# Kernel optimization log

Measured on AMD Instinct MI355X. Metric: run time of the kernel, lower is better.

The kernel has to match this reference:

```python
import jax, jax.numpy as jnp
import numpy as np

B, S, D_IN, D_OUT = 4, 2048, 2048, 8192


def setup_inputs() -> dict:
    key = jax.random.key(0)
    k1, k2 = jax.random.split(key)
    x = jax.random.normal(k1, (B, S, D_IN), dtype=jnp.float32)
    weight = jax.random.normal(k2, (D_OUT, D_IN), dtype=jnp.float32) * 0.02
    alpha = jnp.float32(1.0)
    bias = jnp.zeros((D_OUT,), dtype=jnp.float32)
    return {"x": x, "weight": weight, "alpha": alpha, "bias": bias}


def reference(x, weight, alpha, bias):
    # Ternary quantization: delta = 0.7 * mean(|w|); w_q in {-1,0,1} * alpha
    delta = 0.7 * jnp.mean(jnp.abs(weight))
    w_t = jnp.where(weight > delta, jnp.float32(1.0),
                    jnp.where(weight < -delta, jnp.float32(-1.0), jnp.float32(0.0)))
    w_q = w_t * alpha  # [out, in]
    # F.linear: x @ w_q^T + bias
    return jnp.einsum('bsd,od->bso', x, w_q) + bias
```

## Files before the change

### kernel.cpp

```cpp
#include <hip/hip_runtime.h>
#include <hip/hip_bf16.h>
#include <stdint.h>

typedef __attribute__((ext_vector_type(4))) int i32x4;
typedef __attribute__((ext_vector_type(16))) int i32x16;
typedef signed char s8;

#define M_TOT 8192
#define N_TOT 8192
#define K_TOT 2048
#define W_COUNT (N_TOT * K_TOT)
#define X_COUNT (M_TOT * K_TOT)

__global__ void tl_reduce(const float* __restrict__ w, const float* __restrict__ x,
                          double* __restrict__ wsum, float* __restrict__ xmax) {
    const int b = blockIdx.x;
    if (b < 1024) {
        const int tid = b * 256 + threadIdx.x;
        const float4* w4 = (const float4*)w;
        double s = 0.0;
        for (int i = tid; i < W_COUNT / 4; i += 1024 * 256) {
            float4 v = w4[i];
            s += (double)fabsf(v.x) + (double)fabsf(v.y) + (double)fabsf(v.z) + (double)fabsf(v.w);
        }
        #pragma unroll
        for (int off = 32; off > 0; off >>= 1) s += __shfl_down(s, off);
        __shared__ double red[4];
        if ((threadIdx.x & 63) == 0) red[threadIdx.x >> 6] = s;
        __syncthreads();
        if (threadIdx.x == 0) wsum[b] = (red[0] + red[1]) + (red[2] + red[3]);
    } else {
        const int tid = (b - 1024) * 256 + threadIdx.x;
        const float4* x4 = (const float4*)x;
        float m = 0.0f;
        for (int i = tid; i < X_COUNT / 4; i += 1024 * 256) {
            float4 v = x4[i];
            m = fmaxf(m, fmaxf(fmaxf(fabsf(v.x), fabsf(v.y)), fmaxf(fabsf(v.z), fabsf(v.w))));
        }
        #pragma unroll
        for (int off = 32; off > 0; off >>= 1) m = fmaxf(m, __shfl_down(m, off));
        __shared__ float redm[4];
        if ((threadIdx.x & 63) == 0) redm[threadIdx.x >> 6] = m;
        __syncthreads();
        if (threadIdx.x == 0) xmax[b - 1024] = fmaxf(fmaxf(redm[0], redm[1]), fmaxf(redm[2], redm[3]));
    }
}

__global__ void tl_finalize(const double* __restrict__ wsum, const float* __restrict__ xmax,
                            const float* __restrict__ alpha,
                            double* __restrict__ delta, float* __restrict__ qp) {
    const int t = threadIdx.x;
    double s = (wsum[t] + wsum[t + 256]) + (wsum[t + 512] + wsum[t + 768]);
    float m = fmaxf(fmaxf(xmax[t], xmax[t + 256]), fmaxf(xmax[t + 512], xmax[t + 768]));
    #pragma unroll
    for (int off = 32; off > 0; off >>= 1) {
        s += __shfl_down(s, off);
        m = fmaxf(m, __shfl_down(m, off));
    }
    __shared__ double rs[4];
    __shared__ float rm[4];
    if ((t & 63) == 0) { rs[t >> 6] = s; rm[t >> 6] = m; }
    __syncthreads();
    if (t == 0) {
        *delta = 0.7 * (((rs[0] + rs[1]) + (rs[2] + rs[3])) / (double)W_COUNT);
        float mm = fmaxf(fmaxf(rm[0], rm[1]), fmaxf(rm[2], rm[3]));
        qp[0] = 127.0f / mm;
        qp[1] = alpha[0] * (mm / 127.0f);
    }
}

__global__ void tl_tern_w(const float* __restrict__ w, const double* __restrict__ delta_p,
                          s8* __restrict__ wb) {
    const double d = *delta_p;
    const int i = (blockIdx.x * 256 + threadIdx.x) * 16;
    union { s8 c[16]; i32x4 v; } o;
    #pragma unroll
    for (int j = 0; j < 16; j += 4) {
        float4 v = *(const float4*)(w + i + j);
        float f[4] = {v.x, v.y, v.z, v.w};
        #pragma unroll
        for (int r = 0; r < 4; ++r) {
            double wd = (double)f[r];
            o.c[j + r] = wd > d ? 1 : (wd < -d ? -1 : 0);
        }
    }
    *(i32x4*)(wb + i) = o.v;
}

__global__ void tl_quant_x(const float* __restrict__ x, const float* __restrict__ qp,
                           s8* __restrict__ xb) {
    const float inv = qp[0];
    const int i = (blockIdx.x * 256 + threadIdx.x) * 16;
    union { s8 c[16]; i32x4 v; } o;
    #pragma unroll
    for (int j = 0; j < 16; j += 4) {
        float4 v = *(const float4*)(x + i + j);
        float f[4] = {v.x, v.y, v.z, v.w};
        #pragma unroll
        for (int r = 0; r < 4; ++r) {
            int q = (int)__builtin_rintf(f[r] * inv);
            q = q > 127 ? 127 : (q < -127 ? -127 : q);
            o.c[j + r] = (s8)q;
        }
    }
    *(i32x4*)(xb + i) = o.v;
}


#define SB    __builtin_amdgcn_sched_barrier(0)
#define BARR  __builtin_amdgcn_s_barrier()
#define LGKM6 asm volatile("s_waitcnt lgkmcnt(6)" ::: "memory")
#define LGKM0 asm volatile("s_waitcnt lgkmcnt(0)" ::: "memory")
#define VMW(N) asm volatile("s_waitcnt vmcnt(" #N ")" ::: "memory")
#define PRIO1 __builtin_amdgcn_s_setprio(1)
#define PRIO0 __builtin_amdgcn_s_setprio(0)

#define GLDS(SRC, DOFF) __builtin_amdgcn_global_load_lds(                      \
    (const __attribute__((address_space(1))) void*)(SRC),                      \
    (__attribute__((address_space(3))) void*)(lds + (DOFF)), 16, 0, 0)

#define RD6(AR, BR, S, KK) do {                                                \
    _Pragma("unroll") for (int m_ = 0; m_ < 4; ++m_)                           \
        AR[m_] = *(const i32x4*)(lds + (S) * 16384 + wrOff + m_ * 2048 +       \
                                 (lrd ^ ((KK) * 32)));                         \
    _Pragma("unroll") for (int n_ = 0; n_ < 2; ++n_)                           \
        BR[n_] = *(const i32x4*)(lds + 49152 + (S) * 16384 + wcOff + n_ * 2048 + \
                                 (lrd ^ ((KK) * 32)));                         \
} while (0)

#define MM(AR, BR) do {                                                        \
    _Pragma("unroll") for (int m_ = 0; m_ < 4; ++m_)                           \
    _Pragma("unroll") for (int n_ = 0; n_ < 2; ++n_)                           \
        acc[m_][n_] = __builtin_amdgcn_mfma_i32_32x32x32_i8(                   \
            AR[m_], BR[n_], acc[m_][n_], 0, 0, 0);                             \
} while (0)

#define STG_A(SS, KOFF) do {                                                   \
    GLDS(aSrc + (KOFF), (SS) * 16384 + L);                                     \
    GLDS(aSrc + (KOFF) + 262144, (SS) * 16384 + 8192 + L);                     \
} while (0)
#define STG_B(SS, KOFF) do {                                                   \
    GLDS(bSrc + (KOFF), 49152 + (SS) * 16384 + L);                             \
    GLDS(bSrc + (KOFF) + 262144, 49152 + (SS) * 16384 + 8192 + L);             \
} while (0)

#define KTILE(S, SN, SG, KOFF, DOSTG, GATE, DONEXT) do {                       \
    RD6(aO, bO, S, 1);                                                         \
    SB; LGKM6; SB;                                                             \
    PRIO1; MM(aE, bE); PRIO0; SB;                                              \
    if (DOSTG) { STG_A(SG, KOFF); STG_B(SG, KOFF); }                           \
    SB; LGKM0; SB;                                                             \
    GATE; BARR; SB;                                                            \
    if (DONEXT) RD6(aE, bE, SN, 0);                                            \
    SB;                                                                        \
    PRIO1; MM(aO, bO); PRIO0; SB;                                              \
} while (0)

__global__ __launch_bounds__(512, 2) void tl_gemm_i8(
    const s8* __restrict__ A, const s8* __restrict__ Bm,
    const float* __restrict__ qp, const float* __restrict__ bias,
    float* __restrict__ C) {
    __shared__ __attribute__((aligned(128))) char lds[98304];

    const int t = threadIdx.x;
    const int wid = t >> 6;
    const int l = t & 63;
    const int wr = wid >> 2;
    const int wc = wid & 3;

    const int bid = blockIdx.x;
    const int xc = bid & 7;
    const int j = bid >> 3;
    const int tm = xc * 4 + ((j >> 3) & 3);
    const int tn = (j >> 5) * 8 + (j & 7);
    const int row0 = tm * 256, col0 = tn * 256;

    const int L = t * 16;
    const int off = L ^ (((L >> 7) & 3) << 4);
    const int sr = off >> 6;
    const int kb = off & 63;
    const s8* aSrc = A + (size_t)(row0 + sr) * K_TOT + kb;
    const s8* bSrc = Bm + (size_t)(col0 + sr) * K_TOT + kb;

    const int rl = l & 31, kg = l >> 5;
    const int lrd = rl * 64 + ((kg ^ ((rl >> 1) & 3)) << 4);
    const int wrOff = wr * 8192;
    const int wcOff = wc * 4096;

    i32x16 acc[4][2] = {};
    i32x4 aE[4], bE[2], aO[4], bO[2];

    STG_A(0, 0); STG_B(0, 0);
    STG_A(1, 64); STG_B(1, 64);
    VMW(4); BARR; SB;
    RD6(aE, bE, 0, 0);

    int koff = 128;
    #pragma unroll 1
    for (int i = 0; i < 10; ++i) {
        KTILE(0, 1, 2, koff, 1, VMW(4), 1); koff += 64;
        KTILE(1, 2, 0, koff, 1, VMW(4), 1); koff += 64;
        KTILE(2, 0, 1, koff, 1, VMW(4), 1); koff += 64;
    }
    KTILE(0, 1, 0, 0, 0, VMW(0), 1);
    KTILE(1, 0, 0, 0, 0, (void)0, 0);

    const float osc = qp[1];
    #pragma unroll
    for (int m_ = 0; m_ < 4; ++m_) {
        const int crow = row0 + wr * 128 + m_ * 32 + kg * 4;
        #pragma unroll
        for (int n_ = 0; n_ < 2; ++n_) {
            const int ccol = col0 + wc * 64 + n_ * 32 + rl;
            const float bv = bias[ccol];
            #pragma unroll
            for (int r = 0; r < 16; ++r) {
                const int row = crow + (r & 3) + 8 * (r >> 2);
                C[(size_t)row * N_TOT + ccol] = (float)acc[m_][n_][r] * osc + bv;
            }
        }
    }
}

extern "C" void kernel_launch(void* const* d_in, const int* in_sizes, int n_in,
                              void* d_out, int out_size, void* d_ws, size_t ws_size,
                              hipStream_t stream) {
    const float* x     = (const float*)d_in[0];
    const float* wgt   = (const float*)d_in[1];
    const float* alpha = (const float*)d_in[2];
    const float* bias  = (const float*)d_in[3];
    float* out = (float*)d_out;

    char* ws = (char*)d_ws;
    double* wsum = (double*)ws;
    float* xmax  = (float*)(ws + 8192);
    double* delta = (double*)(ws + 12288);
    float* qp     = (float*)(ws + 12304);
    s8* xb = (s8*)(ws + 16384);
    s8* wb = (s8*)(ws + 16384 + (size_t)X_COUNT);

    tl_reduce<<<2048, 256, 0, stream>>>(wgt, x, wsum, xmax);
    tl_finalize<<<1, 256, 0, stream>>>(wsum, xmax, alpha, delta, qp);
    tl_tern_w<<<W_COUNT / (256 * 16), 256, 0, stream>>>(wgt, delta, wb);
    tl_quant_x<<<X_COUNT / (256 * 16), 256, 0, stream>>>(x, qp, xb);
    tl_gemm_i8<<<(M_TOT / 256) * (N_TOT / 256), 512, 0, stream>>>(xb, wb, qp, bias, out);
}
```

Measured before the change: 207.0 us.

## Pre-swizzle ternary weights into MFMA fragment order and load B directly to registers

The weight ternarization kernel now writes int8 weights in a fragment-major layout that matches the MFMA B-operand register layout. The GEMM loads B straight from global memory into registers, double-buffered, instead of staging it through LDS, which halves the LDS footprint and removes B LDS reads. The wait counts and pipeline schedule are reworked to match. The risk is that B loads now hit global memory and L2 from each wave separately, with no LDS sharing across the four row waves, and the vmcnt accounting becomes harder to keep correct.

```diff
diff --git a/kernel.cpp b/kernel.cpp
--- a/kernel.cpp
+++ b/kernel.cpp
@@ -70,13 +70,17 @@
 }
 
 __global__ void tl_tern_w(const float* __restrict__ w, const double* __restrict__ delta_p,
-                          s8* __restrict__ wb) {
+                          s8* __restrict__ wbF) {
     const double d = *delta_p;
-    const int i = (blockIdx.x * 256 + threadIdx.x) * 16;
+    const int i = blockIdx.x * 256 + threadIdx.x;
+    const int frag = i >> 6, lane = i & 63;
+    const int n = (frag >> 6) * 32 + (lane & 31);
+    const int k = (frag & 63) * 32 + (lane >> 5) * 16;
+    const float* src = w + (size_t)n * K_TOT + k;
     union { s8 c[16]; i32x4 v; } o;
     #pragma unroll
     for (int j = 0; j < 16; j += 4) {
-        float4 v = *(const float4*)(w + i + j);
+        float4 v = *(const float4*)(src + j);
         float f[4] = {v.x, v.y, v.z, v.w};
         #pragma unroll
         for (int r = 0; r < 4; ++r) {
@@ -84,7 +88,7 @@
             o.c[j + r] = wd > d ? 1 : (wd < -d ? -1 : 0);
         }
     }
-    *(i32x4*)(wb + i) = o.v;
+    *(i32x4*)(wbF + (size_t)i * 16) = o.v;
 }
 
 __global__ void tl_quant_x(const float* __restrict__ x, const float* __restrict__ qp,
@@ -109,7 +113,7 @@
 
 #define SB    __builtin_amdgcn_sched_barrier(0)
 #define BARR  __builtin_amdgcn_s_barrier()
-#define LGKM6 asm volatile("s_waitcnt lgkmcnt(6)" ::: "memory")
+#define LGKM4 asm volatile("s_waitcnt lgkmcnt(4)" ::: "memory")
 #define LGKM0 asm volatile("s_waitcnt lgkmcnt(0)" ::: "memory")
 #define VMW(N) asm volatile("s_waitcnt vmcnt(" #N ")" ::: "memory")
 #define PRIO1 __builtin_amdgcn_s_setprio(1)
@@ -119,48 +123,53 @@
     (const __attribute__((address_space(1))) void*)(SRC),                      \
     (__attribute__((address_space(3))) void*)(lds + (DOFF)), 16, 0, 0)
 
-#define RD6(AR, BR, S, KK) do {                                                \
+#define RD_A4(AR, S, KK) do {                                                  \
     _Pragma("unroll") for (int m_ = 0; m_ < 4; ++m_)                           \
         AR[m_] = *(const i32x4*)(lds + (S) * 16384 + wrOff + m_ * 2048 +       \
                                  (lrd ^ ((KK) * 32)));                         \
-    _Pragma("unroll") for (int n_ = 0; n_ < 2; ++n_)                           \
-        BR[n_] = *(const i32x4*)(lds + 49152 + (S) * 16384 + wcOff + n_ * 2048 + \
-                                 (lrd ^ ((KK) * 32)));                         \
-} while (0)
-
-#define MM(AR, BR) do {                                                        \
-    _Pragma("unroll") for (int m_ = 0; m_ < 4; ++m_)                           \
-    _Pragma("unroll") for (int n_ = 0; n_ < 2; ++n_)                           \
-        acc[m_][n_] = __builtin_amdgcn_mfma_i32_32x32x32_i8(                   \
-            AR[m_], BR[n_], acc[m_][n_], 0, 0, 0);                             \
+} while (0)
+
+#define LDB4(BX, BOFF) do {                                                    \
+    BX[0] = *(const i32x4*)(bPtr + (BOFF));                                    \
+    BX[1] = *(const i32x4*)(bPtr + (BOFF) + 1024);                             \
+    BX[2] = *(const i32x4*)(bPtr + (BOFF) + 65536);                            \
+    BX[3] = *(const i32x4*)(bPtr + (BOFF) + 65536 + 1024);                     \
+} while (0)
+
+#define MM8(AX, B0, B1) do {                                                   \
+    _Pragma("unroll") for (int m_ = 0; m_ < 4; ++m_) {                         \
+        acc[m_][0] = __builtin_amdgcn_mfma_i32_32x32x32_i8(AX[m_], B0, acc[m_][0], 0, 0, 0); \
+        acc[m_][1] = __builtin_amdgcn_mfma_i32_32x32x32_i8(AX[m_], B1, acc[m_][1], 0, 0, 0); \
+    }                                                                          \
 } while (0)
 
 #define STG_A(SS, KOFF) do {                                                   \
     GLDS(aSrc + (KOFF), (SS) * 16384 + L);                                     \
     GLDS(aSrc + (KOFF) + 262144, (SS) * 16384 + 8192 + L);                     \
 } while (0)
-#define STG_B(SS, KOFF) do {                                                   \
-    GLDS(bSrc + (KOFF), 49152 + (SS) * 16384 + L);                             \
-    GLDS(bSrc + (KOFF) + 262144, 49152 + (SS) * 16384 + 8192 + L);             \
-} while (0)
-
-#define KTILE(S, SN, SG, KOFF, DOSTG, GATE, DONEXT) do {                       \
-    RD6(aO, bO, S, 1);                                                         \
-    SB; LGKM6; SB;                                                             \
-    PRIO1; MM(aE, bE); PRIO0; SB;                                              \
-    if (DOSTG) { STG_A(SG, KOFF); STG_B(SG, KOFF); }                           \
-    SB; LGKM0; SB;                                                             \
-    GATE; BARR; SB;                                                            \
-    if (DONEXT) RD6(aE, bE, SN, 0);                                            \
+
+#define KT(S, SN, SG, BCUR, BNXT, W1, W2, DOSTG, DOB, DONEXT) do {             \
+    RD_A4(aO, S, 1);                                                           \
+    if (DOB) { LDB4(BNXT, boff); }                                             \
     SB;                                                                        \
-    PRIO1; MM(aO, bO); PRIO0; SB;                                              \
+    if (DOSTG) { STG_A(SG, koff); }                                            \
+    SB;                                                                        \
+    W1; SB;                                                                    \
+    LGKM4; SB;                                                                 \
+    PRIO1; MM8(aE, BCUR[0], BCUR[2]); PRIO0; SB;                               \
+    LGKM0; SB;                                                                 \
+    W2; SB;                                                                    \
+    BARR; SB;                                                                  \
+    if (DONEXT) { RD_A4(aE, SN, 0); SB; }                                      \
+    PRIO1; MM8(aO, BCUR[1], BCUR[3]); PRIO0; SB;                               \
+    koff += 64; boff += 2048;                                                  \
 } while (0)
 
 __global__ __launch_bounds__(512, 2) void tl_gemm_i8(
-    const s8* __restrict__ A, const s8* __restrict__ Bm,
+    const s8* __restrict__ A, const s8* __restrict__ BmF,
     const float* __restrict__ qp, const float* __restrict__ bias,
     float* __restrict__ C) {
-    __shared__ __attribute__((aligned(128))) char lds[98304];
+    __shared__ __attribute__((aligned(128))) char lds[49152];
 
     const int t = threadIdx.x;
     const int wid = t >> 6;
@@ -180,30 +189,36 @@
     const int sr = off >> 6;
     const int kb = off & 63;
     const s8* aSrc = A + (size_t)(row0 + sr) * K_TOT + kb;
-    const s8* bSrc = Bm + (size_t)(col0 + sr) * K_TOT + kb;
+
+    const s8* bPtr = BmF + (size_t)((col0 >> 5) + wc * 2) * 65536 + l * 16;
 
     const int rl = l & 31, kg = l >> 5;
     const int lrd = rl * 64 + ((kg ^ ((rl >> 1) & 3)) << 4);
     const int wrOff = wr * 8192;
-    const int wcOff = wc * 4096;
 
     i32x16 acc[4][2] = {};
-    i32x4 aE[4], bE[2], aO[4], bO[2];
-
-    STG_A(0, 0); STG_B(0, 0);
-    STG_A(1, 64); STG_B(1, 64);
-    VMW(4); BARR; SB;
-    RD6(aE, bE, 0, 0);
+    i32x4 aE[4], aO[4], bC[4], bN[4];
+
+    STG_A(0, 0); SB;
+    LDB4(bC, 0); SB;
+    STG_A(1, 64); SB;
+    VMW(6); SB;
+    BARR; SB;
+    RD_A4(aE, 0, 0); SB;
 
     int koff = 128;
+    int boff = 2048;
     #pragma unroll 1
-    for (int i = 0; i < 10; ++i) {
-        KTILE(0, 1, 2, koff, 1, VMW(4), 1); koff += 64;
-        KTILE(1, 2, 0, koff, 1, VMW(4), 1); koff += 64;
-        KTILE(2, 0, 1, koff, 1, VMW(4), 1); koff += 64;
-    }
-    KTILE(0, 1, 0, 0, 0, VMW(0), 1);
-    KTILE(1, 0, 0, 0, 0, (void)0, 0);
+    for (int i = 0; i < 5; ++i) {
+        KT(0, 1, 2, bC, bN, VMW(8), VMW(6), 1, 1, 1);
+        KT(1, 2, 0, bN, bC, VMW(8), VMW(6), 1, 1, 1);
+        KT(2, 0, 1, bC, bN, VMW(8), VMW(6), 1, 1, 1);
+        KT(0, 1, 2, bN, bC, VMW(8), VMW(6), 1, 1, 1);
+        KT(1, 2, 0, bC, bN, VMW(8), VMW(6), 1, 1, 1);
+        KT(2, 0, 1, bN, bC, VMW(8), VMW(6), 1, 1, 1);
+    }
+    KT(0, 1, 0, bC, bN, VMW(6), VMW(4), 0, 1, 1);
+    KT(1, 0, 0, bN, bC, VMW(0), (void)0, 0, 0, 0);
 
     const float osc = qp[1];
     #pragma unroll
```

Measured after the change: 223.5 us. 1.08x slower.

## Make GEMM persistent over four column tiles and overlap epilogue with next prologue

Applied to the files above, without the earlier changes.

The int8 GEMM now launches 256 blocks, each looping over four output column tiles instead of one tile per block. The epilogue stores for the previous tile are issued after the next tile's first global-to-LDS stages, so the C writes can overlap the prefetch. This targets tail and launch overhead and exposed epilogue latency. In exchange the grid is smaller (256 blocks at two per CU), which may leave CUs idle, and tiles are remapped to new locations.

```diff
diff --git a/kernel.cpp b/kernel.cpp
--- a/kernel.cpp
+++ b/kernel.cpp
@@ -156,6 +156,21 @@
     PRIO1; MM(aO, bO); PRIO0; SB;                                              \
 } while (0)
 
+#define EPI(C0) do {                                                           \
+    _Pragma("unroll") for (int m_ = 0; m_ < 4; ++m_) {                         \
+        const int crow_ = row0 + wr * 128 + m_ * 32 + kg * 4;                  \
+        _Pragma("unroll") for (int n_ = 0; n_ < 2; ++n_) {                     \
+            const int ccol_ = (C0) + wc * 64 + n_ * 32 + rl;                   \
+            const float bv_ = bias[ccol_];                                     \
+            _Pragma("unroll") for (int r_ = 0; r_ < 16; ++r_) {                \
+                const int row_ = crow_ + (r_ & 3) + 8 * (r_ >> 2);             \
+                C[(size_t)row_ * N_TOT + ccol_] =                              \
+                    (float)acc[m_][n_][r_] * osc + bv_;                        \
+            }                                                                  \
+        }                                                                      \
+    }                                                                          \
+} while (0)
+
 __global__ __launch_bounds__(512, 2) void tl_gemm_i8(
     const s8* __restrict__ A, const s8* __restrict__ Bm,
     const float* __restrict__ qp, const float* __restrict__ bias,
@@ -169,57 +184,63 @@
     const int wc = wid & 3;
 
     const int bid = blockIdx.x;
-    const int xc = bid & 7;
-    const int j = bid >> 3;
-    const int tm = xc * 4 + ((j >> 3) & 3);
-    const int tn = (j >> 5) * 8 + (j & 7);
-    const int row0 = tm * 256, col0 = tn * 256;
+    const int xcd = bid & 7;
+    const int bb = bid >> 3;
+    const int tm = xcd * 4 + (bb >> 3);
+    const int tnb = bb & 7;
+    const int row0 = tm * 256;
 
     const int L = t * 16;
     const int off = L ^ (((L >> 7) & 3) << 4);
     const int sr = off >> 6;
     const int kb = off & 63;
     const s8* aSrc = A + (size_t)(row0 + sr) * K_TOT + kb;
-    const s8* bSrc = Bm + (size_t)(col0 + sr) * K_TOT + kb;
 
     const int rl = l & 31, kg = l >> 5;
     const int lrd = rl * 64 + ((kg ^ ((rl >> 1) & 3)) << 4);
     const int wrOff = wr * 8192;
     const int wcOff = wc * 4096;
 
+    const float osc = qp[1];
+    const i32x16 VZ = {};
+
     i32x16 acc[4][2] = {};
     i32x4 aE[4], bE[2], aO[4], bO[2];
 
-    STG_A(0, 0); STG_B(0, 0);
-    STG_A(1, 64); STG_B(1, 64);
-    VMW(4); BARR; SB;
-    RD6(aE, bE, 0, 0);
-
-    int koff = 128;
+    int col0prev = 0;
     #pragma unroll 1
-    for (int i = 0; i < 10; ++i) {
-        KTILE(0, 1, 2, koff, 1, VMW(4), 1); koff += 64;
-        KTILE(1, 2, 0, koff, 1, VMW(4), 1); koff += 64;
-        KTILE(2, 0, 1, koff, 1, VMW(4), 1); koff += 64;
-    }
-    KTILE(0, 1, 0, 0, 0, VMW(0), 1);
-    KTILE(1, 0, 0, 0, 0, (void)0, 0);
-
-    const float osc = qp[1];
-    #pragma unroll
-    for (int m_ = 0; m_ < 4; ++m_) {
-        const int crow = row0 + wr * 128 + m_ * 32 + kg * 4;
-        #pragma unroll
-        for (int n_ = 0; n_ < 2; ++n_) {
-            const int ccol = col0 + wc * 64 + n_ * 32 + rl;
-            const float bv = bias[ccol];
+    for (int r = 0; r < 4; ++r) {
+        const int col0 = (r * 8 + tnb) * 256;
+        const s8* bSrc = Bm + (size_t)(col0 + sr) * K_TOT + kb;
+
+        STG_A(0, 0); STG_B(0, 0);
+        STG_A(1, 64); STG_B(1, 64);
+        if (r > 0) {
+            EPI(col0prev);
+            VMW(63); SB;
+        } else {
+            VMW(4); SB;
+        }
+        BARR; SB;
+        #pragma unroll
+        for (int m_ = 0; m_ < 4; ++m_)
             #pragma unroll
-            for (int r = 0; r < 16; ++r) {
-                const int row = crow + (r & 3) + 8 * (r >> 2);
-                C[(size_t)row * N_TOT + ccol] = (float)acc[m_][n_][r] * osc + bv;
-            }
-        }
-    }
+            for (int n_ = 0; n_ < 2; ++n_) acc[m_][n_] = VZ;
+        RD6(aE, bE, 0, 0); SB;
+
+        int koff = 128;
+        #pragma unroll 1
+        for (int i = 0; i < 10; ++i) {
+            KTILE(0, 1, 2, koff, 1, VMW(4), 1); koff += 64;
+            KTILE(1, 2, 0, koff, 1, VMW(4), 1); koff += 64;
+            KTILE(2, 0, 1, koff, 1, VMW(4), 1); koff += 64;
+        }
+        KTILE(0, 1, 0, 0, 0, VMW(0), 1);
+        KTILE(1, 0, 0, 0, 0, (void)0, 0);
+
+        col0prev = col0;
+    }
+    EPI(col0prev);
 }
 
 extern "C" void kernel_launch(void* const* d_in, const int* in_sizes, int n_in,
@@ -243,5 +264,5 @@
     tl_finalize<<<1, 256, 0, stream>>>(wsum, xmax, alpha, delta, qp);
     tl_tern_w<<<W_COUNT / (256 * 16), 256, 0, stream>>>(wgt, delta, wb);
     tl_quant_x<<<X_COUNT / (256 * 16), 256, 0, stream>>>(x, qp, xb);
-    tl_gemm_i8<<<(M_TOT / 256) * (N_TOT / 256), 512, 0, stream>>>(xb, wb, qp, bias, out);
-}
+    tl_gemm_i8<<<256, 512, 0, stream>>>(xb, wb, qp, bias, out);
+}
```

After: 261.3 us. +26.2%, slower.
